# Kernel tuning notes

Hardware: AMD Instinct MI355X
Metric: run time of the kernel (lower is better)

## Reference

```python
import jax, jax.numpy as jnp
import numpy as np
from jax import lax

T = 3650      # days
H = 256       # MLP hidden width
N_IN = 4      # [s_snow, s_water, prcp, tmean]
N_OUT = 5     # [p_snow, p_rain, m, et, q]
DT = 1.0      # euler step (days), equals forcing sampling interval


def setup_inputs() -> dict:
    key = jax.random.key(0)
    ks = jax.random.split(key, 8)
    # inputs[:, 0]=s_snow init traj, [:,1]=s_water, [:,2]=prcp, [:,3]=tmean, [:,4]=time
    data = jax.random.normal(ks[0], (T, 4), dtype=jnp.float32)
    data = data.at[:, 2].set(jnp.abs(data[:, 2]))  # prcp >= 0
    time = jnp.arange(T, dtype=jnp.float32)[:, None]
    inputs = jnp.concatenate([data, time], axis=-1)  # [T, 5]
    dayl = jax.random.uniform(ks[1], (T,), dtype=jnp.float32)  # day length fraction
    s = 0.1  # small init keeps sinh/exp transforms stable over the long rollout
    W0 = jax.random.normal(ks[2], (N_IN, H), dtype=jnp.float32) * (s / np.sqrt(N_IN))
    b0 = jnp.zeros((H,), dtype=jnp.float32)
    W1 = jax.random.normal(ks[3], (H, H), dtype=jnp.float32) * (s / np.sqrt(H))
    b1 = jnp.zeros((H,), dtype=jnp.float32)
    W2 = jax.random.normal(ks[4], (H, H), dtype=jnp.float32) * (s / np.sqrt(H))
    b2 = jnp.zeros((H,), dtype=jnp.float32)
    Wout = jax.random.normal(ks[5], (H, N_OUT), dtype=jnp.float32) * (s / np.sqrt(H))
    bout = jnp.zeros((N_OUT,), dtype=jnp.float32)
    return {"inputs": inputs, "dayl": dayl, "W0": W0, "b0": b0, "W1": W1,
            "b1": b1, "W2": W2, "b2": b2, "Wout": Wout, "bout": bout}


def _step_function(x):
    return (jnp.tanh(5.0 * x) + 1.0) * 0.5


def reference(inputs, dayl, W0, b0, W1, b1, W2, b2, Wout, bout):
    prcp = inputs[:, 2]
    tmean = inputs[:, 3]
    s_snow0 = inputs[0, 0]
    s_water0 = inputs[0, 1]

    def mlp(x):  # x: [..., N_IN] -> [..., N_OUT]
        h = jnp.tanh(x @ W0 + b0)
        h = jnp.tanh(h @ W1 + b1)
        h = jnpp_tanh(h @ W2 + b2) if False else jnp.tanh(h @ W2 + b2)
        return h @ Wout + bout

    def derivs(s0, s1, p, tm, ld):
        o = mlp(jnp.stack([s0, s1, p, tm]))  # [5]
        p_snow, p_rain, m, et, q = o[0], o[1], o[2], o[3], o[4]
        # scale_target_vars transform path
        p_snow = jax.nn.relu(jnp.sinh(p_snow) * _step_function(-tm))
        p_rain = jax.nn.relu(jnp.sinh(p_rain))
        m = jax.nn.relu(_step_function(s0) * jnp.sinh(m))
        et = _step_function(s1) * jnp.exp(et) * ld
        q = _step_function(s1) * jnp.exp(q)
        return p_snow - m, p_rain + m - et - q

    def body(carry, xs):
        s0, s1 = carry
        p, tm, ld = xs
        d0, d1 = derivs(s0, s1, p, tm, ld)
        ns0 = s0 + DT * d0
        ns1 = s1 + DT * d1
        return (ns0, ns1), (ns0, ns1)

    xs = (prcp[:-1], tmean[:-1], dayl[:-1])
    _, (ss, sw) = lax.scan(body, (s_snow0, s_water0), xs)
    s_snow_nn = jnp.concatenate([s_snow0[None], ss])    # [T]
    s_water_nn = jnp.concatenate([s_water0[None], sw])  # [T]

    inputs_nn = jnp.stack([s_snow_nn, s_water_nn, prcp, tmean], axis=-1)  # [T, 4]
    q_output = mlp(inputs_nn)[:, -1]  # last head = q
    return (q_output, s_snow_nn, s_water_nn)
```

## Files before the change

### kernel.cpp

```cpp
#include <hip/hip_runtime.h>
#include <hip/hip_bf16.h>

#define TT 3650
#define HH 256
#define LDS_PAD 10240

typedef _Float16 f16x8 __attribute__((ext_vector_type(8)));
typedef float f32x4 __attribute__((ext_vector_type(4)));

__device__ __forceinline__ float xexp2(float x) { return __builtin_amdgcn_exp2f(x); }
__device__ __forceinline__ float xrcp(float x) { return __builtin_amdgcn_rcpf(x); }
__device__ __forceinline__ float xexp(float x) { return xexp2(x * 1.4426950408889634f); }
__device__ __forceinline__ float xtanh(float x) {
  float e = xexp2(x * 2.8853900817779268f);
  return 1.0f - 2.0f * xrcp(e + 1.0f);
}
__device__ __forceinline__ float xstep(float x) {
  return xrcp(1.0f + xexp2(-14.426950408889634f * x));
}
__device__ __forceinline__ float xsinh(float x) {
  float e = xexp(x);
  return 0.5f * (e - xrcp(e));
}

#define DPPADD(x, ctrl)                                                        \
  (x) += __builtin_bit_cast(float, __builtin_amdgcn_update_dpp(                \
            0, __builtin_bit_cast(int, (x)), (ctrl), 0xf, 0xf, false));

#define REP8(M) M(0) M(1) M(2) M(3) M(4) M(5) M(6) M(7)

#define WSCALE 1024.0f
#define WDESCALE 0.0009765625f

__global__ void __launch_bounds__(512) exphydro_scan(
    const float* __restrict__ gin, const float* __restrict__ gdayl,
    const float* __restrict__ gW0, const float* __restrict__ gb0,
    const float* __restrict__ gW1, const float* __restrict__ gb1,
    const float* __restrict__ gW2, const float* __restrict__ gb2,
    const float* __restrict__ gWout, const float* __restrict__ gbout,
    float* __restrict__ gout) {
  __shared__ alignas(16) _Float16 h0l[HH];
  __shared__ alignas(16) _Float16 h1l[HH];
  __shared__ float sWP[64];
  __shared__ float sP[TT], sTm[TT];
  __shared__ float sLd[TT + LDS_PAD];

  const int tid = threadIdx.x;
  const int lane = tid & 63;
  const int w = tid >> 6;
  const int li = lane & 15;
  const int g = lane >> 4;
  const int jA = 32 * w + li;
  const int jB = jA + 16;

  for (int i = tid; i < TT; i += 512) {
    sP[i] = gin[5 * i + 2];
    sTm[i] = gin[5 * i + 3];
    sLd[i] = gdayl[i];
  }
  if (tid < 64) sWP[tid] = 0.0f;

  float s0 = gin[0], s1 = gin[1];
  const float bo0 = gbout[0], bo1 = gbout[1], bo2 = gbout[2], bo3 = gbout[3],
              bo4 = gbout[4];
  const float w0A0 = gW0[jA], w0A1 = gW0[HH + jA], w0A2 = gW0[2 * HH + jA],
              w0A3 = gW0[3 * HH + jA];
  const float w0B0 = gW0[jB], w0B1 = gW0[HH + jB], w0B2 = gW0[2 * HH + jB],
              w0B3 = gW0[3 * HH + jB];
  const float b0A = gb0[jA], b0B = gb0[jB], b1A = gb1[jA], b1B = gb1[jB],
              b2A = gb2[jA], b2B = gb2[jB];
  const float woA0 = gWout[5 * jA + 0], woA1 = gWout[5 * jA + 1],
              woA2 = gWout[5 * jA + 2], woA3 = gWout[5 * jA + 3],
              woA4 = gWout[5 * jA + 4];
  const float woB0 = gWout[5 * jB + 0], woB1 = gWout[5 * jB + 1],
              woB2 = gWout[5 * jB + 2], woB3 = gWout[5 * jB + 3],
              woB4 = gWout[5 * jB + 4];

#define FDECL(i) f16x8 a1A_##i, a1B_##i, a2A_##i, a2B_##i;
  REP8(FDECL)
#undef FDECL
#define MK(dst, G, i, j)                                                       \
  {                                                                            \
    const float* p = (G) + (32 * (i) + g * 8) * HH + (j);                      \
    f16x8 f;                                                                   \
    f[0] = (_Float16)(p[0] * WSCALE);      f[1] = (_Float16)(p[HH] * WSCALE);  \
    f[2] = (_Float16)(p[2 * HH] * WSCALE); f[3] = (_Float16)(p[3 * HH] * WSCALE); \
    f[4] = (_Float16)(p[4 * HH] * WSCALE); f[5] = (_Float16)(p[5 * HH] * WSCALE); \
    f[6] = (_Float16)(p[6 * HH] * WSCALE); f[7] = (_Float16)(p[7 * HH] * WSCALE); \
    dst = f;                                                                   \
    asm volatile("" : "+a"(dst));                                              \
  }
#define FINIT(i) MK(a1A_##i, gW1, i, jA) MK(a1B_##i, gW1, i, jB)               \
                 MK(a2A_##i, gW2, i, jA) MK(a2B_##i, gW2, i, jB)
  REP8(FINIT)
#undef FINIT
#undef MK

  const char* hp0 = (const char*)h0l + g * 16;
  const char* hp1 = (const char*)h1l + g * 16;

  __syncthreads();

  for (int t = 0; t < TT; ++t) {
    const float p_in = sP[t];
    const float tm = sTm[t];
    const float ld = sLd[t];

    float h0A = xtanh(b0A + s0 * w0A0 + s1 * w0A1 + p_in * w0A2 + tm * w0A3);
    float h0B = xtanh(b0B + s0 * w0B0 + s1 * w0B1 + p_in * w0B2 + tm * w0B3);
    if (lane < 16) {
      h0l[jA] = (_Float16)h0A;
      h0l[jB] = (_Float16)h0B;
    }
    __syncthreads();

    f32x4 dA = {0.f, 0.f, 0.f, 0.f}, dB = {0.f, 0.f, 0.f, 0.f};
    asm volatile("s_nop 1" : "+v"(dA), "+v"(dB));
#define MM1(i)                                                                 \
  {                                                                            \
    f16x8 av = *(const f16x8*)(hp0 + (i) * 64);                                \
    asm("v_mfma_f32_16x16x32_f16 %0, %1, %2, %0"                               \
        : "+v"(dA) : "v"(av), "a"(a1A_##i));                                   \
    asm("v_mfma_f32_16x16x32_f16 %0, %1, %2, %0"                               \
        : "+v"(dB) : "v"(av), "a"(a1B_##i));                                   \
  }
    REP8(MM1)
#undef MM1
    asm volatile("s_nop 7\n\ts_nop 7" : "+v"(dA), "+v"(dB));
    float h1A = xtanh(dA[0] * WDESCALE + b1A);
    float h1B = xtanh(dB[0] * WDESCALE + b1B);
    if (lane < 16) {
      h1l[jA] = (_Float16)h1A;
      h1l[jB] = (_Float16)h1B;
    }
    __syncthreads();

    f32x4 eA = {0.f, 0.f, 0.f, 0.f}, eB = {0.f, 0.f, 0.f, 0.f};
    asm volatile("s_nop 1" : "+v"(eA), "+v"(eB));
#define MM2(i)                                                                 \
  {                                                                            \
    f16x8 av = *(const f16x8*)(hp1 + (i) * 64);                                \
    asm("v_mfma_f32_16x16x32_f16 %0, %1, %2, %0"                               \
        : "+v"(eA) : "v"(av), "a"(a2A_##i));                                   \
    asm("v_mfma_f32_16x16x32_f16 %0, %1, %2, %0"                               \
        : "+v"(eB) : "v"(av), "a"(a2B_##i));                                   \
  }
    REP8(MM2)
#undef MM2
    asm volatile("s_nop 7\n\ts_nop 7" : "+v"(eA), "+v"(eB));
    float h2A = xtanh(eA[0] * WDESCALE + b2A);
    float h2B = xtanh(eB[0] * WDESCALE + b2B);

    float p0 = h2A * woA0 + h2B * woB0;
    float p1 = h2A * woA1 + h2B * woB1;
    float p2 = h2A * woA2 + h2B * woB2;
    float p3 = h2A * woA3 + h2B * woB3;
    float p4 = h2A * woA4 + h2B * woB4;
    DPPADD(p0, 0x121) DPPADD(p0, 0x122) DPPADD(p0, 0x124) DPPADD(p0, 0x128)
    DPPADD(p1, 0x121) DPPADD(p1, 0x122) DPPADD(p1, 0x124) DPPADD(p1, 0x128)
    DPPADD(p2, 0x121) DPPADD(p2, 0x122) DPPADD(p2, 0x124) DPPADD(p2, 0x128)
    DPPADD(p3, 0x121) DPPADD(p3, 0x122) DPPADD(p3, 0x124) DPPADD(p3, 0x128)
    DPPADD(p4, 0x121) DPPADD(p4, 0x122) DPPADD(p4, 0x124) DPPADD(p4, 0x128)
    if (lane == 0) {
      sWP[w * 8 + 0] = p0; sWP[w * 8 + 1] = p1; sWP[w * 8 + 2] = p2;
      sWP[w * 8 + 3] = p3; sWP[w * 8 + 4] = p4;
    }
    __syncthreads();

    float v = sWP[lane];
    DPPADD(v, 0x128)
    v += __builtin_bit_cast(
        float, __builtin_amdgcn_ds_swizzle(__builtin_bit_cast(int, v), 0x401F));
    float o0 = __builtin_bit_cast(float, __builtin_amdgcn_readlane(__builtin_bit_cast(int, v), 0)) +
               __builtin_bit_cast(float, __builtin_amdgcn_readlane(__builtin_bit_cast(int, v), 32)) + bo0;
    float o1 = __builtin_bit_cast(float, __builtin_amdgcn_readlane(__builtin_bit_cast(int, v), 1)) +
               __builtin_bit_cast(float, __builtin_amdgcn_readlane(__builtin_bit_cast(int, v), 33)) + bo1;
    float o2 = __builtin_bit_cast(float, __builtin_amdgcn_readlane(__builtin_bit_cast(int, v), 2)) +
               __builtin_bit_cast(float, __builtin_amdgcn_readlane(__builtin_bit_cast(int, v), 34)) + bo2;
    float o3 = __builtin_bit_cast(float, __builtin_amdgcn_readlane(__builtin_bit_cast(int, v), 3)) +
               __builtin_bit_cast(float, __builtin_amdgcn_readlane(__builtin_bit_cast(int, v), 35)) + bo3;
    float o4 = __builtin_bit_cast(float, __builtin_amdgcn_readlane(__builtin_bit_cast(int, v), 4)) +
               __builtin_bit_cast(float, __builtin_amdgcn_readlane(__builtin_bit_cast(int, v), 36)) + bo4;
    if (tid == 0) {
      gout[t] = o4;
      gout[TT + t] = s0;
      gout[2 * TT + t] = s1;
    }
    float sh0 = xsinh(o0), sh1 = xsinh(o1), sh2 = xsinh(o2);
    float e3 = xexp(o3), e4 = xexp(o4);
    float stn = xstep(-tm), st0 = xstep(s0), st1 = xstep(s1);
    float psn = fmaxf(sh0 * stn, 0.0f);
    float prn = fmaxf(sh1, 0.0f);
    float mm = fmaxf(st0 * sh2, 0.0f);
    float evt = st1 * e3 * ld;
    float qq = st1 * e4;
    s0 += psn - mm;
    s1 += prn + mm - evt - qq;
  }
}

extern "C" void kernel_launch(void* const* d_in, const int* in_sizes, int n_in,
                              void* d_out, int out_size, void* d_ws, size_t ws_size,
                              hipStream_t stream) {
  const float* gin   = (const float*)d_in[0];
  const float* gdayl = (const float*)d_in[1];
  const float* gW0   = (const float*)d_in[2];
  const float* gb0   = (const float*)d_in[3];
  const float* gW1   = (const float*)d_in[4];
  const float* gb1   = (const float*)d_in[5];
  const float* gW2   = (const float*)d_in[6];
  const float* gb2   = (const float*)d_in[7];
  const float* gWout = (const float*)d_in[8];
  const float* gbout = (const float*)d_in[9];
  float* gout = (float*)d_out;
  exphydro_scan<<<dim3(1), dim3(512), 0, stream>>>(
      gin, gdayl, gW0, gb0, gW1, gb1, gW2, gb2, gWout, gbout, gout);
}
```

Measured before the change: 5.235 ms.

## Halve block to four waves, each computing four output columns per step

The block shrinks from 8 to 4 wavefronts, and each wave now keeps four 16-column MFMA weight slices in AGPRs instead of two, so each lane produces four hidden units. The intent is cheaper __syncthreads barriers and a shorter cross-wave reduction on the serial per-timestep critical path. The final reduction now uses a transposed sWP layout with quad DPP adds, and the three forcing arrays are packed into one f32x4 LDS array, so each step needs a single LDS load. The trade-off is more serial MFMA and tanh work per wave, plus higher AGPR and VGPR pressure.

New measurement: 4.956 ms. 1.06x faster.

```diff
diff --git a/kernel.cpp b/kernel.cpp
--- a/kernel.cpp
+++ b/kernel.cpp
@@ -3,8 +3,8 @@
 
 #define TT 3650
 #define HH 256
-#define LDS_PAD 10240
-
+
+typedef _Float16 f16x4 __attribute__((ext_vector_type(4)));
 typedef _Float16 f16x8 __attribute__((ext_vector_type(8)));
 typedef float f32x4 __attribute__((ext_vector_type(4)));
 
@@ -26,13 +26,19 @@
 #define DPPADD(x, ctrl)                                                        \
   (x) += __builtin_bit_cast(float, __builtin_amdgcn_update_dpp(                \
             0, __builtin_bit_cast(int, (x)), (ctrl), 0xf, 0xf, false));
+#define RDLANE(x, l)                                                           \
+  __builtin_bit_cast(float,                                                    \
+      __builtin_amdgcn_readlane(__builtin_bit_cast(int, (x)), (l)))
 
 #define REP8(M) M(0) M(1) M(2) M(3) M(4) M(5) M(6) M(7)
+#define REPC(M) M(0) M(1) M(2) M(3)
 
 #define WSCALE 1024.0f
 #define WDESCALE 0.0009765625f
 
-__global__ void __launch_bounds__(512) exphydro_scan(
+#define SF_PAD 1500
+
+__global__ void __launch_bounds__(256, 1) exphydro_scan(
     const float* __restrict__ gin, const float* __restrict__ gdayl,
     const float* __restrict__ gW0, const float* __restrict__ gb0,
     const float* __restrict__ gW1, const float* __restrict__ gb1,
@@ -42,46 +48,44 @@
   __shared__ alignas(16) _Float16 h0l[HH];
   __shared__ alignas(16) _Float16 h1l[HH];
   __shared__ float sWP[64];
-  __shared__ float sP[TT], sTm[TT];
-  __shared__ float sLd[TT + LDS_PAD];
+  __shared__ f32x4 sF[TT + SF_PAD];
 
   const int tid = threadIdx.x;
   const int lane = tid & 63;
   const int w = tid >> 6;
   const int li = lane & 15;
   const int g = lane >> 4;
-  const int jA = 32 * w + li;
-  const int jB = jA + 16;
-
-  for (int i = tid; i < TT; i += 512) {
-    sP[i] = gin[5 * i + 2];
-    sTm[i] = gin[5 * i + 3];
-    sLd[i] = gdayl[i];
+  const int jb = 64 * w + 4 * li;
+
+  for (int i = tid; i < TT; i += 256) {
+    f32x4 F = {gin[5 * i + 2], gin[5 * i + 3], gdayl[i], 0.0f};
+    sF[i] = F;
   }
   if (tid < 64) sWP[tid] = 0.0f;
 
   float s0 = gin[0], s1 = gin[1];
   const float bo0 = gbout[0], bo1 = gbout[1], bo2 = gbout[2], bo3 = gbout[3],
               bo4 = gbout[4];
-  const float w0A0 = gW0[jA], w0A1 = gW0[HH + jA], w0A2 = gW0[2 * HH + jA],
-              w0A3 = gW0[3 * HH + jA];
-  const float w0B0 = gW0[jB], w0B1 = gW0[HH + jB], w0B2 = gW0[2 * HH + jB],
-              w0B3 = gW0[3 * HH + jB];
-  const float b0A = gb0[jA], b0B = gb0[jB], b1A = gb1[jA], b1B = gb1[jB],
-              b2A = gb2[jA], b2B = gb2[jB];
-  const float woA0 = gWout[5 * jA + 0], woA1 = gWout[5 * jA + 1],
-              woA2 = gWout[5 * jA + 2], woA3 = gWout[5 * jA + 3],
-              woA4 = gWout[5 * jA + 4];
-  const float woB0 = gWout[5 * jB + 0], woB1 = gWout[5 * jB + 1],
-              woB2 = gWout[5 * jB + 2], woB3 = gWout[5 * jB + 3],
-              woB4 = gWout[5 * jB + 4];
-
-#define FDECL(i) f16x8 a1A_##i, a1B_##i, a2A_##i, a2B_##i;
+#define CDECL(c)                                                               \
+  const float w00_##c = gW0[jb + (c)], w01_##c = gW0[HH + jb + (c)],           \
+              w02_##c = gW0[2 * HH + jb + (c)],                                \
+              w03_##c = gW0[3 * HH + jb + (c)], b0_##c = gb0[jb + (c)],        \
+              b1_##c = gb1[jb + (c)], b2_##c = gb2[jb + (c)],                  \
+              wo0_##c = gWout[5 * (jb + (c)) + 0],                             \
+              wo1_##c = gWout[5 * (jb + (c)) + 1],                             \
+              wo2_##c = gWout[5 * (jb + (c)) + 2],                             \
+              wo3_##c = gWout[5 * (jb + (c)) + 3],                             \
+              wo4_##c = gWout[5 * (jb + (c)) + 4];
+  REPC(CDECL)
+#undef CDECL
+
+#define FDECL(i) f16x8 a1_0_##i, a1_1_##i, a1_2_##i, a1_3_##i,                 \
+                       a2_0_##i, a2_1_##i, a2_2_##i, a2_3_##i;
   REP8(FDECL)
 #undef FDECL
-#define MK(dst, G, i, j)                                                       \
+#define MK(dst, G, i, c)                                                       \
   {                                                                            \
-    const float* p = (G) + (32 * (i) + g * 8) * HH + (j);                      \
+    const float* p = (G) + (32 * (i) + g * 8) * HH + jb + (c);                 \
     f16x8 f;                                                                   \
     f[0] = (_Float16)(p[0] * WSCALE);      f[1] = (_Float16)(p[HH] * WSCALE);  \
     f[2] = (_Float16)(p[2 * HH] * WSCALE); f[3] = (_Float16)(p[3 * HH] * WSCALE); \
@@ -90,8 +94,11 @@
     dst = f;                                                                   \
     asm volatile("" : "+a"(dst));                                              \
   }
-#define FINIT(i) MK(a1A_##i, gW1, i, jA) MK(a1B_##i, gW1, i, jB)               \
-                 MK(a2A_##i, gW2, i, jA) MK(a2B_##i, gW2, i, jB)
+#define FINIT(i)                                                               \
+  MK(a1_0_##i, gW1, i, 0) MK(a1_1_##i, gW1, i, 1)                              \
+  MK(a1_2_##i, gW1, i, 2) MK(a1_3_##i, gW1, i, 3)                              \
+  MK(a2_0_##i, gW2, i, 0) MK(a2_1_##i, gW2, i, 1)                              \
+  MK(a2_2_##i, gW2, i, 2) MK(a2_3_##i, gW2, i, 3)
   REP8(FINIT)
 #undef FINIT
 #undef MK
@@ -99,104 +106,107 @@
   const char* hp0 = (const char*)h0l + g * 16;
   const char* hp1 = (const char*)h1l + g * 16;
 
+#define MFMA(acc, a, b)                                                        \
+  asm("v_mfma_f32_16x16x32_f16 %0, %1, %2, %0" : "+v"(acc) : "v"(a), "a"(b));
+
   __syncthreads();
 
   for (int t = 0; t < TT; ++t) {
-    const float p_in = sP[t];
-    const float tm = sTm[t];
-    const float ld = sLd[t];
-
-    float h0A = xtanh(b0A + s0 * w0A0 + s1 * w0A1 + p_in * w0A2 + tm * w0A3);
-    float h0B = xtanh(b0B + s0 * w0B0 + s1 * w0B1 + p_in * w0B2 + tm * w0B3);
+    f32x4 F = sF[t];
+    const float p_in = F[0];
+    const float tm = F[1];
+    const float ld = F[2];
+
+#define L0C(c)                                                                 \
+  float h0_##c =                                                               \
+      xtanh(b0_##c + s0 * w00_##c + s1 * w01_##c + p_in * w02_##c + tm * w03_##c);
+    REPC(L0C)
+#undef L0C
     if (lane < 16) {
-      h0l[jA] = (_Float16)h0A;
-      h0l[jB] = (_Float16)h0B;
+      f16x4 hv = {(_Float16)h0_0, (_Float16)h0_1, (_Float16)h0_2,
+                  (_Float16)h0_3};
+      *(f16x4*)((char*)h0l + (jb << 1)) = hv;
     }
     __syncthreads();
 
-    f32x4 dA = {0.f, 0.f, 0.f, 0.f}, dB = {0.f, 0.f, 0.f, 0.f};
-    asm volatile("s_nop 1" : "+v"(dA), "+v"(dB));
+    f32x4 d0 = {0.f, 0.f, 0.f, 0.f}, d1 = {0.f, 0.f, 0.f, 0.f};
+    f32x4 d2 = {0.f, 0.f, 0.f, 0.f}, d3 = {0.f, 0.f, 0.f, 0.f};
+    asm volatile("s_nop 1" : "+v"(d0), "+v"(d1), "+v"(d2), "+v"(d3));
 #define MM1(i)                                                                 \
   {                                                                            \
     f16x8 av = *(const f16x8*)(hp0 + (i) * 64);                                \
-    asm("v_mfma_f32_16x16x32_f16 %0, %1, %2, %0"                               \
-        : "+v"(dA) : "v"(av), "a"(a1A_##i));                                   \
-    asm("v_mfma_f32_16x16x32_f16 %0, %1, %2, %0"                               \
-        : "+v"(dB) : "v"(av), "a"(a1B_##i));                                   \
+    MFMA(d0, av, a1_0_##i) MFMA(d1, av, a1_1_##i)                              \
+    MFMA(d2, av, a1_2_##i) MFMA(d3, av, a1_3_##i)                              \
   }
     REP8(MM1)
 #undef MM1
-    asm volatile("s_nop 7\n\ts_nop 7" : "+v"(dA), "+v"(dB));
-    float h1A = xtanh(dA[0] * WDESCALE + b1A);
-    float h1B = xtanh(dB[0] * WDESCALE + b1B);
+    asm volatile("s_nop 7\n\ts_nop 7" : "+v"(d0), "+v"(d1), "+v"(d2), "+v"(d3));
+#define H1C(c) float h1_##c = xtanh(d##c[0] * WDESCALE + b1_##c);
+    REPC(H1C)
+#undef H1C
     if (lane < 16) {
-      h1l[jA] = (_Float16)h1A;
-      h1l[jB] = (_Float16)h1B;
+      f16x4 hv = {(_Float16)h1_0, (_Float16)h1_1, (_Float16)h1_2,
+                  (_Float16)h1_3};
+      *(f16x4*)((char*)h1l + (jb << 1)) = hv;
     }
     __syncthreads();
 
-    f32x4 eA = {0.f, 0.f, 0.f, 0.f}, eB = {0.f, 0.f, 0.f, 0.f};
-    asm volatile("s_nop 1" : "+v"(eA), "+v"(eB));
+    f32x4 e0 = {0.f, 0.f, 0.f, 0.f}, e1 = {0.f, 0.f, 0.f, 0.f};
+    f32x4 e2 = {0.f, 0.f, 0.f, 0.f}, e3 = {0.f, 0.f, 0.f, 0.f};
+    asm volatile("s_nop 1" : "+v"(e0), "+v"(e1), "+v"(e2), "+v"(e3));
 #define MM2(i)                                                                 \
   {                                                                            \
     f16x8 av = *(const f16x8*)(hp1 + (i) * 64);                                \
-    asm("v_mfma_f32_16x16x32_f16 %0, %1, %2, %0"                               \
-        : "+v"(eA) : "v"(av), "a"(a2A_##i));                                   \
-    asm("v_mfma_f32_16x16x32_f16 %0, %1, %2, %0"                               \
-        : "+v"(eB) : "v"(av), "a"(a2B_##i));                                   \
+    MFMA(e0, av, a2_0_##i) MFMA(e1, av, a2_1_##i)                              \
+    MFMA(e2, av, a2_2_##i) MFMA(e3, av, a2_3_##i)                              \
   }
     REP8(MM2)
 #undef MM2
-    asm volatile("s_nop 7\n\ts_nop 7" : "+v"(eA), "+v"(eB));
-    float h2A = xtanh(eA[0] * WDESCALE + b2A);
-    float h2B = xtanh(eB[0] * WDESCALE + b2B);
-
-    float p0 = h2A * woA0 + h2B * woB0;
-    float p1 = h2A * woA1 + h2B * woB1;
-    float p2 = h2A * woA2 + h2B * woB2;
-    float p3 = h2A * woA3 + h2B * woB3;
-    float p4 = h2A * woA4 + h2B * woB4;
+    asm volatile("s_nop 7\n\ts_nop 7" : "+v"(e0), "+v"(e1), "+v"(e2), "+v"(e3));
+#define H2C(c) float h2_##c = xtanh(e##c[0] * WDESCALE + b2_##c);
+    REPC(H2C)
+#undef H2C
+
+    float p0 = h2_0 * wo0_0 + h2_1 * wo0_1 + h2_2 * wo0_2 + h2_3 * wo0_3;
+    float p1 = h2_0 * wo1_0 + h2_1 * wo1_1 + h2_2 * wo1_2 + h2_3 * wo1_3;
+    float p2 = h2_0 * wo2_0 + h2_1 * wo2_1 + h2_2 * wo2_2 + h2_3 * wo2_3;
+    float p3 = h2_0 * wo3_0 + h2_1 * wo3_1 + h2_2 * wo3_2 + h2_3 * wo3_3;
+    float p4 = h2_0 * wo4_0 + h2_1 * wo4_1 + h2_2 * wo4_2 + h2_3 * wo4_3;
     DPPADD(p0, 0x121) DPPADD(p0, 0x122) DPPADD(p0, 0x124) DPPADD(p0, 0x128)
     DPPADD(p1, 0x121) DPPADD(p1, 0x122) DPPADD(p1, 0x124) DPPADD(p1, 0x128)
     DPPADD(p2, 0x121) DPPADD(p2, 0x122) DPPADD(p2, 0x124) DPPADD(p2, 0x128)
     DPPADD(p3, 0x121) DPPADD(p3, 0x122) DPPADD(p3, 0x124) DPPADD(p3, 0x128)
     DPPADD(p4, 0x121) DPPADD(p4, 0x122) DPPADD(p4, 0x124) DPPADD(p4, 0x128)
-    if (lane == 0) {
-      sWP[w * 8 + 0] = p0; sWP[w * 8 + 1] = p1; sWP[w * 8 + 2] = p2;
-      sWP[w * 8 + 3] = p3; sWP[w * 8 + 4] = p4;
-    }
+    float pv = lane == 0 ? p0 : lane == 1 ? p1 : lane == 2 ? p2
+                                          : lane == 3 ? p3 : p4;
+    if (lane < 5) sWP[lane * 4 + w] = pv;
     __syncthreads();
 
     float v = sWP[lane];
-    DPPADD(v, 0x128)
-    v += __builtin_bit_cast(
-        float, __builtin_amdgcn_ds_swizzle(__builtin_bit_cast(int, v), 0x401F));
-    float o0 = __builtin_bit_cast(float, __builtin_amdgcn_readlane(__builtin_bit_cast(int, v), 0)) +
-               __builtin_bit_cast(float, __builtin_amdgcn_readlane(__builtin_bit_cast(int, v), 32)) + bo0;
-    float o1 = __builtin_bit_cast(float, __builtin_amdgcn_readlane(__builtin_bit_cast(int, v), 1)) +
-               __builtin_bit_cast(float, __builtin_amdgcn_readlane(__builtin_bit_cast(int, v), 33)) + bo1;
-    float o2 = __builtin_bit_cast(float, __builtin_amdgcn_readlane(__builtin_bit_cast(int, v), 2)) +
-               __builtin_bit_cast(float, __builtin_amdgcn_readlane(__builtin_bit_cast(int, v), 34)) + bo2;
-    float o3 = __builtin_bit_cast(float, __builtin_amdgcn_readlane(__builtin_bit_cast(int, v), 3)) +
-               __builtin_bit_cast(float, __builtin_amdgcn_readlane(__builtin_bit_cast(int, v), 35)) + bo3;
-    float o4 = __builtin_bit_cast(float, __builtin_amdgcn_readlane(__builtin_bit_cast(int, v), 4)) +
-               __builtin_bit_cast(float, __builtin_amdgcn_readlane(__builtin_bit_cast(int, v), 36)) + bo4;
+    DPPADD(v, 0xB1)
+    DPPADD(v, 0x4E)
+    float o0 = RDLANE(v, 0) + bo0;
+    float o1 = RDLANE(v, 4) + bo1;
+    float o2 = RDLANE(v, 8) + bo2;
+    float o3 = RDLANE(v, 12) + bo3;
+    float o4 = RDLANE(v, 16) + bo4;
     if (tid == 0) {
       gout[t] = o4;
       gout[TT + t] = s0;
       gout[2 * TT + t] = s1;
     }
     float sh0 = xsinh(o0), sh1 = xsinh(o1), sh2 = xsinh(o2);
-    float e3 = xexp(o3), e4 = xexp(o4);
+    float e3x = xexp(o3), e4x = xexp(o4);
     float stn = xstep(-tm), st0 = xstep(s0), st1 = xstep(s1);
     float psn = fmaxf(sh0 * stn, 0.0f);
     float prn = fmaxf(sh1, 0.0f);
     float mm = fmaxf(st0 * sh2, 0.0f);
-    float evt = st1 * e3 * ld;
-    float qq = st1 * e4;
+    float evt = st1 * e3x * ld;
+    float qq = st1 * e4x;
     s0 += psn - mm;
     s1 += prn + mm - evt - qq;
   }
+#undef MFMA
 }
 
 extern "C" void kernel_launch(void* const* d_in, const int* in_sizes, int n_in,
@@ -213,6 +223,6 @@
   const float* gWout = (const float*)d_in[8];
   const float* gbout = (const float*)d_in[9];
   float* gout = (float*)d_out;
-  exphydro_scan<<<dim3(1), dim3(512), 0, stream>>>(
+  exphydro_scan<<<dim3(1), dim3(256), 0, stream>>>(
       gin, gdayl, gW0, gb0, gW1, gb1, gW2, gb2, gWout, gbout, gout);
 }
```
